# Optimization experiments

Measured on AMD Instinct MI355X. Metric: run time of the kernel, lower is better.

Reference implementation:

```python
import jax, jax.numpy as jnp
import numpy as np

B, D, C = 4096, 2048, 64
L_HP, D_HP, OMEGA, EPSILON = 0.5, 1.0, 100.0, 0.1
LN_EPS = 1e-5
CLASS_COUNTS = [5000,4500,4050,3645,3280,2952,2657,2391,2152,1937,1743,1569,1412,1271,1144,1029,926,834,750,675,608,547,492,443,399,359,323,291,262,236,212,191,172,155,139,125,113,101,91,82,74,66,60,54,48,43,39,35,32,28,26,23,21,19,17,15,14,12,11,10,9,8,7,7]


def setup_inputs() -> dict:
    key = jax.random.key(0)
    k_x, k_y, k_b, k_u1, k_u2 = jax.random.split(key, 5)
    counts = jnp.asarray(CLASS_COUNTS, dtype=jnp.float32)
    # set_class_weights: tilde_C = 1/log(counts*d + eps), min-max normalized, scaled by l
    tilde = 1.0 / jnp.log(counts * D_HP + EPSILON)
    c = (tilde - jnp.min(tilde)) / (jnp.max(tilde) - jnp.min(tilde)) * L_HP
    # set_fs_classes: 1 where count <= omega
    fs_classes = jnp.where(counts <= OMEGA, 1, 0).astype(jnp.int32)
    x = jax.random.normal(k_x, (B, D), dtype=jnp.float32)
    y = jax.random.randint(k_y, (B,), 0, C)
    beta_idx = jax.random.randint(k_b, (B,), 0, B)
    u1 = jax.random.uniform(k_u1, (B,))
    u2 = jax.random.uniform(k_u2, (B,))
    alpha = jnp.where(u1 > 0.5, u2, jnp.ones((B,), jnp.float32))
    return {"x": x, "y": y, "alpha": alpha, "beta_idx": beta_idx, "c": c, "fs_classes": fs_classes}


def reference(x, y, alpha, beta_idx, c, fs_classes):
    n_batch, dim = x.shape
    num_classes = c.shape[0]
    # --- reconstruct ---
    mu = jnp.mean(x, axis=-1, keepdims=True)
    var = jnp.mean((x - mu) ** 2, axis=-1, keepdims=True)
    x_norm = (x - mu) / jnp.sqrt(var + LN_EPS) / jnp.sqrt(jnp.asarray(dim, x.dtype))
    sim = jnp.matmul(x_norm, x_norm.T)  # [B, B]
    # E[i, j] = eye[i, j] + fs_mask[j]  (broadcast over rows), thresholded to {0, 1}
    fs_mask = fs_classes[y].astype(x.dtype)  # [B]
    E = jnp.eye(n_batch, dtype=x.dtype) + fs_mask[None, :]
    E = jnp.where(E >= 1.0, 1.0, 0.0)
    sim = jax.nn.softmax(sim - 100000.0 * E, axis=-1)
    contrib = c[y]  # [B]
    reconstructions = jnp.matmul(sim, x)  # [B, D]
    R = reconstructions * contrib[:, None] + x * (1.0 - contrib)[:, None]
    # --- pairwise_mix: M @ R with M[i,:] = alpha[i]*e_i + (1-alpha[i])*e_{beta_idx[i]} ---
    y_oh = jax.nn.one_hot(y, num_classes, dtype=x.dtype)
    a = alpha[:, None]
    x_mix = a * R + (1.0 - a) * R[beta_idx]
    y_mix = a * y_oh + (1.0 - a) * y_oh[beta_idx]
    return (x_mix, y_mix)
```

## Files before the change

### kernel.cpp

```cpp
#include <hip/hip_runtime.h>
#include <cstdint>
#include <cstddef>

typedef __bf16 bf16;
typedef __bf16 bf16x4 __attribute__((ext_vector_type(4)));
typedef __bf16 bf16x8 __attribute__((ext_vector_type(8)));
typedef float floatx4 __attribute__((ext_vector_type(4)));
typedef int intx8 __attribute__((ext_vector_type(8)));

#define NB 4096
#define ND 2048
#define NCLS 64
#define TSTRIDE 144
#define OS 136

__device__ __forceinline__ void stage16(const void* g, void* l) {
  __builtin_amdgcn_global_load_lds(
      (__attribute__((address_space(1))) unsigned int*)g,
      (__attribute__((address_space(3))) unsigned int*)l, 16, 0, 0);
}

__device__ __forceinline__ unsigned char fp8x1(float f) {
  return (unsigned char)(__builtin_amdgcn_cvt_pk_fp8_f32(f, f, 0, false) & 0xFF);
}
__device__ __forceinline__ int fp8x4(float f0, float f1, float f2, float f3) {
  int d = __builtin_amdgcn_cvt_pk_fp8_f32(f0, f1, 0, false);
  return __builtin_amdgcn_cvt_pk_fp8_f32(f2, f3, d, true);
}

__device__ __forceinline__ void stage_step(const unsigned char* __restrict__ A,
                                           const unsigned char* __restrict__ B,
                                           int K, int m0, int n0, int k0,
                                           unsigned char* As,
                                           unsigned char* Bs) {
  const int t = threadIdx.x;
  const int w = t >> 6, lane = t & 63;
#pragma unroll
  for (int q = 0; q < 4; ++q) {
    const int slot = w * 256 + q * 64 + lane;
    const int row = slot >> 3;
    const int cc = (slot & 7) ^ (row & 7);
    stage16(A + (size_t)(m0 + row) * K + (k0 + cc * 16),
            As + (w * 256 + q * 64) * 16);
  }
#pragma unroll
  for (int q = 0; q < 4; ++q) {
    const int slot = w * 256 + q * 64 + lane;
    const int row = slot >> 3;
    const int cc = (slot & 7) ^ (row & 7);
    stage16(B + (size_t)(n0 + row) * K + (k0 + cc * 16),
            Bs + (w * 256 + q * 64) * 16);
  }
}

#define READ_A(i)                                                       \
  {                                                                     \
    const int row = wm * 64 + (i)*16 + lm;                              \
    const int c0 = (quad * 2) ^ (row & 7);                              \
    const int4 lo = *(const int4*)(Ac + row * 128 + c0 * 16);           \
    const int4 hi = *(const int4*)(Ac + row * 128 + (c0 ^ 1) * 16);     \
    af[i][0] = lo.x; af[i][1] = lo.y; af[i][2] = lo.z; af[i][3] = lo.w; \
    af[i][4] = hi.x; af[i][5] = hi.y; af[i][6] = hi.z; af[i][7] = hi.w; \
  }
#define READ_B(i)                                                            \
  {                                                                          \
    const int row = wn * 64 + (i)*16 + lm;                                   \
    const int c0 = (quad * 2) ^ (row & 7);                                   \
    const int4 lo = *(const int4*)(Bc + row * 128 + c0 * 16);                \
    const int4 hi = *(const int4*)(Bc + row * 128 + (c0 ^ 1) * 16);          \
    bfr[i][0] = lo.x; bfr[i][1] = lo.y; bfr[i][2] = lo.z; bfr[i][3] = lo.w;  \
    bfr[i][4] = hi.x; bfr[i][5] = hi.y; bfr[i][6] = hi.z; bfr[i][7] = hi.w;  \
  }
#define MFMA(mi, ni)                                                \
  acc[mi][ni] = __builtin_amdgcn_mfma_scale_f32_16x16x128_f8f6f4(   \
      af[mi], bfr[ni], acc[mi][ni], 0, 0, 0, 127, 0, 127)

__device__ __forceinline__ void gemm_core8(const unsigned char* __restrict__ A,
                                           const unsigned char* __restrict__ B,
                                           int K, int m0, int n0,
                                           unsigned char* As0, unsigned char* Bs0,
                                           unsigned char* As1, unsigned char* Bs1,
                                           floatx4 acc[4][4]) {
  const int t = threadIdx.x;
  const int w = t >> 6;
  const int lane = t & 63;
  const int wm = w >> 1, wn = w & 1;
  const int lm = lane & 15, quad = lane >> 4;
  const int nk = K >> 7;

  stage_step(A, B, K, m0, n0, 0, As0, Bs0);

  for (int k = 0; k < nk; ++k) {
    __syncthreads();
    if (k + 1 < nk)
      stage_step(A, B, K, m0, n0, (k + 1) << 7, (k & 1) ? As0 : As1,
                 (k & 1) ? Bs0 : Bs1);
    unsigned char* Ac = (k & 1) ? As1 : As0;
    unsigned char* Bc = (k & 1) ? Bs1 : Bs0;

    intx8 af[4], bfr[4];
    READ_A(0); READ_A(1); READ_B(0); READ_B(1);
    MFMA(0, 0); MFMA(0, 1); MFMA(1, 0); MFMA(1, 1);
    READ_A(2); READ_A(3);
    MFMA(2, 0); MFMA(2, 1); MFMA(3, 0); MFMA(3, 1);
    READ_B(2); READ_B(3);
    MFMA(0, 2); MFMA(0, 3); MFMA(1, 2); MFMA(1, 3);
    MFMA(2, 2); MFMA(2, 3); MFMA(3, 2); MFMA(3, 3);
  }
}


__global__ __launch_bounds__(256) void prep_kernel(
    const float* __restrict__ x, const int* __restrict__ y,
    const float* __restrict__ alpha, const int* __restrict__ beta_idx,
    const float* __restrict__ c, const int* __restrict__ fs,
    unsigned char* __restrict__ XN8, unsigned char* __restrict__ XBT8,
    bf16* __restrict__ XB16, float* __restrict__ lrow,
    float* __restrict__ contrib, int* __restrict__ maskcol,
    float* __restrict__ out) {
  __shared__ float tile[64][65];
  const int t = threadIdx.x;

  if (blockIdx.x < NB) {
    const int row = blockIdx.x;
    const float4* xr = (const float4*)(x + (size_t)row * ND);
    float4 v0 = xr[t], v1 = xr[t + 256];
    float s = v0.x + v0.y + v0.z + v0.w + v1.x + v1.y + v1.z + v1.w;
    float q = v0.x * v0.x + v0.y * v0.y + v0.z * v0.z + v0.w * v0.w +
              v1.x * v1.x + v1.y * v1.y + v1.z * v1.z + v1.w * v1.w;
#pragma unroll
    for (int o = 32; o > 0; o >>= 1) {
      s += __shfl_down(s, o);
      q += __shfl_down(q, o);
    }
    const int w = t >> 6;
    if ((t & 63) == 0) { tile[0][w] = s; tile[1][w] = q; }
    __syncthreads();
    s = tile[0][0] + tile[0][1] + tile[0][2] + tile[0][3];
    q = tile[1][0] + tile[1][1] + tile[1][2] + tile[1][3];
    const float mu = s * (1.0f / ND);
    const float var = q * (1.0f / ND) - mu * mu;
    const float sc =
        rsqrtf(var + 1e-5f) * 0.02209708691207961f * 32.0f;

    int* orow = (int*)(XN8 + (size_t)row * ND);
    orow[t] = fp8x4((v0.x - mu) * sc, (v0.y - mu) * sc, (v0.z - mu) * sc,
                    (v0.w - mu) * sc);
    orow[256 + t] = fp8x4((v1.x - mu) * sc, (v1.y - mu) * sc, (v1.z - mu) * sc,
                          (v1.w - mu) * sc);

    bf16x4 b0, b1;
    b0[0] = (bf16)v0.x; b0[1] = (bf16)v0.y; b0[2] = (bf16)v0.z; b0[3] = (bf16)v0.w;
    b1[0] = (bf16)v1.x; b1[1] = (bf16)v1.y; b1[2] = (bf16)v1.z; b1[3] = (bf16)v1.w;
    *(bf16x4*)(XB16 + (size_t)row * ND + t * 4) = b0;
    *(bf16x4*)(XB16 + (size_t)row * ND + 1024 + t * 4) = b1;

    if (t == 0) {
      lrow[row] = 0.0f;
      const int yi = y[row];
      contrib[row] = c[yi];
      maskcol[row] = fs[yi];
    }
  } else if (blockIdx.x < NB + 2048) {
    const int b2 = blockIdx.x - NB;
    const int rb = b2 & 63;
    const int cb = b2 >> 6;
    const int tx = t & 63, ty = t >> 6;
#pragma unroll
    for (int rr = ty; rr < 64; rr += 4)
      tile[rr][tx] = x[(size_t)(rb * 64 + rr) * ND + cb * 64 + tx];
    __syncthreads();
    const int ro = t >> 2;
    const int co = t & 3;
    int4 v;
    {
      const int j = co * 16;
      v.x = fp8x4(tile[j + 0][ro], tile[j + 1][ro], tile[j + 2][ro], tile[j + 3][ro]);
      v.y = fp8x4(tile[j + 4][ro], tile[j + 5][ro], tile[j + 6][ro], tile[j + 7][ro]);
      v.z = fp8x4(tile[j + 8][ro], tile[j + 9][ro], tile[j + 10][ro], tile[j + 11][ro]);
      v.w = fp8x4(tile[j + 12][ro], tile[j + 13][ro], tile[j + 14][ro], tile[j + 15][ro]);
    }
    *(int4*)(XBT8 + (size_t)(cb * 64 + ro) * NB + rb * 64 + co * 16) = v;
  } else {
    const int b3 = blockIdx.x - (NB + 2048);
    const int row = b3 * 4 + (t >> 6);
    const int cls = t & 63;
    const float a = alpha[row];
    const int bi = beta_idx[row];
    const int yi = y[row], yb = y[bi];
    out[(size_t)NB * ND + (size_t)row * NCLS + cls] =
        a * (cls == yi ? 1.0f : 0.0f) + (1.0f - a) * (cls == yb ? 1.0f : 0.0f);
  }
}

__global__ __launch_bounds__(256) void gemm_sim_kernel(
    const unsigned char* __restrict__ XN8, unsigned char* __restrict__ P8,
    float* __restrict__ lrow, const int* __restrict__ maskcol) {
  __shared__ unsigned char smem[65536];
  unsigned char* As0 = smem;
  unsigned char* Bs0 = smem + 16384;
  unsigned char* As1 = smem + 32768;
  unsigned char* Bs1 = smem + 49152;

  const int b = blockIdx.x;
  int bj = (int)((sqrtf(8.0f * (float)b + 1.0f) - 1.0f) * 0.5f);
  while ((bj + 1) * (bj + 2) / 2 <= b) ++bj;
  while (bj * (bj + 1) / 2 > b) --bj;
  const int bi = b - bj * (bj + 1) / 2;
  const int m0 = bi * 128, n0 = bj * 128;

  floatx4 acc[4][4];
#pragma unroll
  for (int i = 0; i < 4; ++i)
#pragma unroll
    for (int j = 0; j < 4; ++j) acc[i][j] = 0.0f;

  gemm_core8(XN8, XN8, ND, m0, n0, As0, Bs0, As1, Bs1, acc);

  const int t = threadIdx.x, w = t >> 6, lane = t & 63;
  const int wm = w >> 1, wn = w & 1, lm = lane & 15, quad = lane >> 4;

  int cmj[4];
#pragma unroll
  for (int ni = 0; ni < 4; ++ni) cmj[ni] = maskcol[n0 + wn * 64 + ni * 16 + lm];
  int rmk[4][4];
#pragma unroll
  for (int mi = 0; mi < 4; ++mi)
#pragma unroll
    for (int r = 0; r < 4; ++r)
      rmk[mi][r] = maskcol[m0 + wm * 64 + mi * 16 + quad * 4 + r];

  float rs[4][4];
#pragma unroll
  for (int mi = 0; mi < 4; ++mi)
#pragma unroll
    for (int r = 0; r < 4; ++r) rs[mi][r] = 0.0f;

#pragma unroll
  for (int ni = 0; ni < 4; ++ni) {
    const int gcol = n0 + wn * 64 + ni * 16 + lm;
#pragma unroll
    for (int mi = 0; mi < 4; ++mi) {
#pragma unroll
      for (int r = 0; r < 4; ++r) {
        const int grow = m0 + wm * 64 + mi * 16 + quad * 4 + r;
        float e = (grow == gcol) ? 0.0f
                                 : __expf(acc[mi][ni][r] * 0.0009765625f);
        acc[mi][ni][r] = e;
        rs[mi][r] += cmj[ni] ? 0.0f : e;
      }
    }
  }
#pragma unroll
  for (int mi = 0; mi < 4; ++mi)
#pragma unroll
    for (int r = 0; r < 4; ++r) {
      float vsum = rs[mi][r];
      vsum += __shfl_xor(vsum, 1);
      vsum += __shfl_xor(vsum, 2);
      vsum += __shfl_xor(vsum, 4);
      vsum += __shfl_xor(vsum, 8);
      if (lm == 0)
        atomicAdd(&lrow[m0 + wm * 64 + mi * 16 + quad * 4 + r], vsum);
    }

  __syncthreads();
#pragma unroll
  for (int ni = 0; ni < 4; ++ni) {
    const int col = wn * 64 + ni * 16 + lm;
#pragma unroll
    for (int mi = 0; mi < 4; ++mi)
#pragma unroll
      for (int r = 0; r < 4; ++r) {
        const int row = wm * 64 + mi * 16 + quad * 4 + r;
        smem[row * TSTRIDE + col] = fp8x1(cmj[ni] ? 0.0f : acc[mi][ni][r]);
      }
  }
  __syncthreads();
#pragma unroll
  for (int it = 0; it < 4; ++it) {
    const int row = it * 32 + (t >> 3), ch = t & 7;
    int4 v = *(const int4*)(smem + row * TSTRIDE + ch * 16);
    *(int4*)(P8 + (size_t)(m0 + row) * NB + n0 + ch * 16) = v;
  }

  if (bi != bj) {
    __syncthreads();
#pragma unroll
    for (int ni = 0; ni < 4; ++ni) {
      const int tc = wn * 64 + ni * 16 + lm;
      float cs = 0.0f;
#pragma unroll
      for (int mi = 0; mi < 4; ++mi) {
        float g0 = rmk[mi][0] ? 0.0f : acc[mi][ni][0];
        float g1 = rmk[mi][1] ? 0.0f : acc[mi][ni][1];
        float g2 = rmk[mi][2] ? 0.0f : acc[mi][ni][2];
        float g3 = rmk[mi][3] ? 0.0f : acc[mi][ni][3];
        cs += g0 + g1 + g2 + g3;
        *(int*)(smem + tc * TSTRIDE + wm * 64 + mi * 16 + quad * 4) =
            fp8x4(g0, g1, g2, g3);
      }
      cs += __shfl_xor(cs, 16);
      cs += __shfl_xor(cs, 32);
      if (quad == 0) atomicAdd(&lrow[n0 + tc], cs);
    }
    __syncthreads();
#pragma unroll
    for (int it = 0; it < 4; ++it) {
      const int row = it * 32 + (t >> 3), ch = t & 7;
      int4 v = *(const int4*)(smem + row * TSTRIDE + ch * 16);
      *(int4*)(P8 + (size_t)(n0 + row) * NB + m0 + ch * 16) = v;
    }
  }
}

__global__ __launch_bounds__(256) void gemm_recon_kernel(
    const unsigned char* __restrict__ P8, const unsigned char* __restrict__ XBT8,
    const bf16* __restrict__ XB16, const float* __restrict__ lrow,
    const float* __restrict__ contrib, bf16* __restrict__ R) {
  __shared__ unsigned char smem[65536];
  unsigned char* As0 = smem;
  unsigned char* Bs0 = smem + 16384;
  unsigned char* As1 = smem + 32768;
  unsigned char* Bs1 = smem + 49152;

  const int id = blockIdx.x;
  const int xcd = id & 7;
  const int s = id >> 3;
  const int bx = xcd * 2 + (s & 1);
  const int by = s >> 1;
  const int m0 = by * 128, n0 = bx * 128;

  floatx4 acc[4][4];
#pragma unroll
  for (int i = 0; i < 4; ++i)
#pragma unroll
    for (int j = 0; j < 4; ++j) acc[i][j] = 0.0f;

  gemm_core8(P8, XBT8, NB, m0, n0, As0, Bs0, As1, Bs1, acc);

  const int t = threadIdx.x, w = t >> 6, lane = t & 63;
  const int wm = w >> 1, wn = w & 1, lm = lane & 15, quad = lane >> 4;

  __syncthreads();
  bf16* osm = (bf16*)smem;
#pragma unroll
  for (int mi = 0; mi < 4; ++mi) {
#pragma unroll
    for (int r = 0; r < 4; ++r) {
      const int lrow_i = wm * 64 + mi * 16 + quad * 4 + r;
      const int grow = m0 + lrow_i;
      const float inv = 1.0f / lrow[grow];
      const float ci = contrib[grow];
#pragma unroll
      for (int ni = 0; ni < 4; ++ni) {
        const int lcol = wn * 64 + ni * 16 + lm;
        const float rec = acc[mi][ni][r] * inv;
        const float xv = (float)XB16[(size_t)grow * ND + n0 + lcol];
        osm[lrow_i * OS + lcol] = (bf16)(rec * ci + xv * (1.0f - ci));
      }
    }
  }
  __syncthreads();
#pragma unroll
  for (int it = 0; it < 8; ++it) {
    const int row = it * 16 + (t >> 4), ch = t & 15;
    int4 v = *(const int4*)(osm + row * OS + ch * 8);
    *(int4*)(R + (size_t)(m0 + row) * ND + n0 + ch * 8) = v;
  }
}

__global__ __launch_bounds__(256) void mix_kernel(
    const bf16* __restrict__ R, const float* __restrict__ alpha,
    const int* __restrict__ beta_idx, float* __restrict__ out) {
  const int i = blockIdx.x, t = threadIdx.x;
  const float a = alpha[i];
  const int bi = beta_idx[i];
  const bf16x8* Ri = (const bf16x8*)(R + (size_t)i * ND);
  const bf16x8* Rb = (const bf16x8*)(R + (size_t)bi * ND);
  const float b = 1.0f - a;
  bf16x8 r = Ri[t], g = Rb[t];
  float4 o0, o1;
  o0.x = a * (float)r[0] + b * (float)g[0];
  o0.y = a * (float)r[1] + b * (float)g[1];
  o0.z = a * (float)r[2] + b * (float)g[2];
  o0.w = a * (float)r[3] + b * (float)g[3];
  o1.x = a * (float)r[4] + b * (float)g[4];
  o1.y = a * (float)r[5] + b * (float)g[5];
  o1.z = a * (float)r[6] + b * (float)g[6];
  o1.w = a * (float)r[7] + b * (float)g[7];
  float4* o = (float4*)(out + (size_t)i * ND + t * 8);
  o[0] = o0;
  o[1] = o1;
}

extern "C" void kernel_launch(void* const* d_in, const int* in_sizes, int n_in,
                              void* d_out, int out_size, void* d_ws,
                              size_t ws_size, hipStream_t stream) {
  const float* x = (const float*)d_in[0];
  const int* y = (const int*)d_in[1];
  const float* alpha = (const float*)d_in[2];
  const int* beta = (const int*)d_in[3];
  const float* c = (const float*)d_in[4];
  const int* fs = (const int*)d_in[5];
  float* out = (float*)d_out;
  char* ws = (char*)d_ws;

  unsigned char* XN8  = (unsigned char*)(ws + 0);
  unsigned char* XBT8 = (unsigned char*)(ws + 8388608);
  unsigned char* P8   = (unsigned char*)(ws + 16777216);
  bf16* R    = (bf16*)(ws + 33554432);
  bf16* XB16 = (bf16*)(ws + 50331648);
  float* LR = (float*)(ws + 67108864);
  float* CT = (float*)(ws + 67108864 + 16384);
  int* MC   = (int*)(ws + 67108864 + 32768);

  prep_kernel<<<NB + 2048 + 1024, 256, 0, stream>>>(x, y, alpha, beta, c, fs,
                                                    XN8, XBT8, XB16, LR, CT,
                                                    MC, out);
  gemm_sim_kernel<<<528, 256, 0, stream>>>(XN8, P8, LR, MC);
  gemm_recon_kernel<<<512, 256, 0, stream>>>(P8, XBT8, XB16, LR, CT, R);
  mix_kernel<<<NB, 256, 0, stream>>>(R, alpha, beta, out);
}
```

Baseline: 180.1 us.

## Load GEMM B operand directly into registers instead of staging through LDS

The B tiles of both FP8 GEMMs are now read straight from global memory into MFMA register fragments, double-buffered in registers, while only A stays staged through LDS. The main loop is unrolled by two with explicit ping-pong buffers. This halves LDS usage per block, which may raise occupancy and cut LDS traffic. In exchange each B element is loaded from global once per wave rather than once per block, and register pressure rises from holding two B fragment sets.

```diff
diff --git a/kernel.cpp b/kernel.cpp
--- a/kernel.cpp
+++ b/kernel.cpp
@@ -28,11 +28,9 @@
   return __builtin_amdgcn_cvt_pk_fp8_f32(f2, f3, d, true);
 }
 
-__device__ __forceinline__ void stage_step(const unsigned char* __restrict__ A,
-                                           const unsigned char* __restrict__ B,
-                                           int K, int m0, int n0, int k0,
-                                           unsigned char* As,
-                                           unsigned char* Bs) {
+__device__ __forceinline__ void stage_a(const unsigned char* __restrict__ A,
+                                        int K, int m0, int k0,
+                                        unsigned char* As) {
   const int t = threadIdx.x;
   const int w = t >> 6, lane = t & 63;
 #pragma unroll
@@ -43,43 +41,48 @@
     stage16(A + (size_t)(m0 + row) * K + (k0 + cc * 16),
             As + (w * 256 + q * 64) * 16);
   }
-#pragma unroll
-  for (int q = 0; q < 4; ++q) {
-    const int slot = w * 256 + q * 64 + lane;
-    const int row = slot >> 3;
-    const int cc = (slot & 7) ^ (row & 7);
-    stage16(B + (size_t)(n0 + row) * K + (k0 + cc * 16),
-            Bs + (w * 256 + q * 64) * 16);
-  }
-}
-
-#define READ_A(i)                                                       \
-  {                                                                     \
-    const int row = wm * 64 + (i)*16 + lm;                              \
-    const int c0 = (quad * 2) ^ (row & 7);                              \
-    const int4 lo = *(const int4*)(Ac + row * 128 + c0 * 16);           \
-    const int4 hi = *(const int4*)(Ac + row * 128 + (c0 ^ 1) * 16);     \
-    af[i][0] = lo.x; af[i][1] = lo.y; af[i][2] = lo.z; af[i][3] = lo.w; \
-    af[i][4] = hi.x; af[i][5] = hi.y; af[i][6] = hi.z; af[i][7] = hi.w; \
-  }
-#define READ_B(i)                                                            \
-  {                                                                          \
-    const int row = wn * 64 + (i)*16 + lm;                                   \
-    const int c0 = (quad * 2) ^ (row & 7);                                   \
-    const int4 lo = *(const int4*)(Bc + row * 128 + c0 * 16);                \
-    const int4 hi = *(const int4*)(Bc + row * 128 + (c0 ^ 1) * 16);          \
-    bfr[i][0] = lo.x; bfr[i][1] = lo.y; bfr[i][2] = lo.z; bfr[i][3] = lo.w;  \
-    bfr[i][4] = hi.x; bfr[i][5] = hi.y; bfr[i][6] = hi.z; bfr[i][7] = hi.w;  \
-  }
-#define MFMA(mi, ni)                                                \
-  acc[mi][ni] = __builtin_amdgcn_mfma_scale_f32_16x16x128_f8f6f4(   \
-      af[mi], bfr[ni], acc[mi][ni], 0, 0, 0, 127, 0, 127)
+}
+
+__device__ __forceinline__ void load_b(const unsigned char* __restrict__ B,
+                                       int K, int n0, int k0, int wn, int lm,
+                                       int quad, intx8 b[4]) {
+#pragma unroll
+  for (int i = 0; i < 4; ++i) {
+    const unsigned char* p =
+        B + (size_t)(n0 + wn * 64 + i * 16 + lm) * K + k0 + quad * 32;
+    const int4 lo = *(const int4*)(p);
+    const int4 hi = *(const int4*)(p + 16);
+    b[i][0] = lo.x; b[i][1] = lo.y; b[i][2] = lo.z; b[i][3] = lo.w;
+    b[i][4] = hi.x; b[i][5] = hi.y; b[i][6] = hi.z; b[i][7] = hi.w;
+  }
+}
+
+__device__ __forceinline__ void half_step(const unsigned char* Ac,
+                                          const intx8 b[4], floatx4 acc[4][4],
+                                          int wm, int lm, int quad) {
+  intx8 af[4];
+#pragma unroll
+  for (int i = 0; i < 4; ++i) {
+    const int row = wm * 64 + i * 16 + lm;
+    const int c0 = (quad * 2) ^ (row & 7);
+    const int4 lo = *(const int4*)(Ac + row * 128 + c0 * 16);
+    const int4 hi = *(const int4*)(Ac + row * 128 + (c0 ^ 1) * 16);
+    af[i][0] = lo.x; af[i][1] = lo.y; af[i][2] = lo.z; af[i][3] = lo.w;
+    af[i][4] = hi.x; af[i][5] = hi.y; af[i][6] = hi.z; af[i][7] = hi.w;
+  }
+#pragma unroll
+  for (int mi = 0; mi < 4; ++mi)
+#pragma unroll
+    for (int ni = 0; ni < 4; ++ni)
+      acc[mi][ni] = __builtin_amdgcn_mfma_scale_f32_16x16x128_f8f6f4(
+          af[mi], b[ni], acc[mi][ni], 0, 0, 0, 127, 0, 127);
+}
 
 __device__ __forceinline__ void gemm_core8(const unsigned char* __restrict__ A,
                                            const unsigned char* __restrict__ B,
                                            int K, int m0, int n0,
-                                           unsigned char* As0, unsigned char* Bs0,
-                                           unsigned char* As1, unsigned char* Bs1,
+                                           unsigned char* As0,
+                                           unsigned char* As1,
                                            floatx4 acc[4][4]) {
   const int t = threadIdx.x;
   const int w = t >> 6;
@@ -88,24 +91,21 @@
   const int lm = lane & 15, quad = lane >> 4;
   const int nk = K >> 7;
 
-  stage_step(A, B, K, m0, n0, 0, As0, Bs0);
-
-  for (int k = 0; k < nk; ++k) {
-    __syncthreads();
-    if (k + 1 < nk)
-      stage_step(A, B, K, m0, n0, (k + 1) << 7, (k & 1) ? As0 : As1,
-                 (k & 1) ? Bs0 : Bs1);
-    unsigned char* Ac = (k & 1) ? As1 : As0;
-    unsigned char* Bc = (k & 1) ? Bs1 : Bs0;
-
-    intx8 af[4], bfr[4];
-    READ_A(0); READ_A(1); READ_B(0); READ_B(1);
-    MFMA(0, 0); MFMA(0, 1); MFMA(1, 0); MFMA(1, 1);
-    READ_A(2); READ_A(3);
-    MFMA(2, 0); MFMA(2, 1); MFMA(3, 0); MFMA(3, 1);
-    READ_B(2); READ_B(3);
-    MFMA(0, 2); MFMA(0, 3); MFMA(1, 2); MFMA(1, 3);
-    MFMA(2, 2); MFMA(2, 3); MFMA(3, 2); MFMA(3, 3);
+  intx8 b0[4], b1[4];
+  stage_a(A, K, m0, 0, As0);
+  load_b(B, K, n0, 0, wn, lm, quad, b0);
+
+  for (int k2 = 0; k2 < nk; k2 += 2) {
+    __syncthreads();
+    stage_a(A, K, m0, (k2 + 1) << 7, As1);
+    load_b(B, K, n0, (k2 + 1) << 7, wn, lm, quad, b1);
+    half_step(As0, b0, acc, wm, lm, quad);
+    __syncthreads();
+    if (k2 + 2 < nk) {
+      stage_a(A, K, m0, (k2 + 2) << 7, As0);
+      load_b(B, K, n0, (k2 + 2) << 7, wn, lm, quad, b0);
+    }
+    half_step(As1, b1, acc, wm, lm, quad);
   }
 }
 
@@ -196,11 +196,9 @@
 __global__ __launch_bounds__(256) void gemm_sim_kernel(
     const unsigned char* __restrict__ XN8, unsigned char* __restrict__ P8,
     float* __restrict__ lrow, const int* __restrict__ maskcol) {
-  __shared__ unsigned char smem[65536];
+  __shared__ unsigned char smem[32768];
   unsigned char* As0 = smem;
-  unsigned char* Bs0 = smem + 16384;
-  unsigned char* As1 = smem + 32768;
-  unsigned char* Bs1 = smem + 49152;
+  unsigned char* As1 = smem + 16384;
 
   const int b = blockIdx.x;
   int bj = (int)((sqrtf(8.0f * (float)b + 1.0f) - 1.0f) * 0.5f);
@@ -215,7 +213,7 @@
 #pragma unroll
     for (int j = 0; j < 4; ++j) acc[i][j] = 0.0f;
 
-  gemm_core8(XN8, XN8, ND, m0, n0, As0, Bs0, As1, Bs1, acc);
+  gemm_core8(XN8, XN8, ND, m0, n0, As0, As1, acc);
 
   const int t = threadIdx.x, w = t >> 6, lane = t & 63;
   const int wm = w >> 1, wn = w & 1, lm = lane & 15, quad = lane >> 4;
@@ -318,11 +316,9 @@
     const unsigned char* __restrict__ P8, const unsigned char* __restrict__ XBT8,
     const bf16* __restrict__ XB16, const float* __restrict__ lrow,
     const float* __restrict__ contrib, bf16* __restrict__ R) {
-  __shared__ unsigned char smem[65536];
+  __shared__ unsigned char smem[34816];
   unsigned char* As0 = smem;
-  unsigned char* Bs0 = smem + 16384;
-  unsigned char* As1 = smem + 32768;
-  unsigned char* Bs1 = smem + 49152;
+  unsigned char* As1 = smem + 16384;
 
   const int id = blockIdx.x;
   const int xcd = id & 7;
@@ -337,7 +333,7 @@
 #pragma unroll
     for (int j = 0; j < 4; ++j) acc[i][j] = 0.0f;
 
-  gemm_core8(P8, XBT8, NB, m0, n0, As0, Bs0, As1, Bs1, acc);
+  gemm_core8(P8, XBT8, NB, m0, n0, As0, As1, acc);
 
   const int t = threadIdx.x, w = t >> 6, lane = t & 63;
   const int wm = w >> 1, wn = w & 1, lm = lane & 15, quad = lane >> 4;
```

Result: slower. 276.3 us (+53.4%).
